# Performance work log

Measured on AMD Instinct MI355X. Metric: run time of the kernel, lower is better.

## Reference

```python
import jax, jax.numpy as jnp
import numpy as np
import math

B, T, C = 4, 2048, 1024
N_HEADS = 16
D_HEAD = C // N_HEADS


def _rope_tables(d_head, max_seq_len):
    half = d_head // 2
    theta = 1.0 / (10000.0 ** (jnp.arange(half, dtype=jnp.float32) / half))
    pos = jnp.arange(max_seq_len, dtype=jnp.float32)
    freqs = jnp.outer(pos, theta)  # [S, half]
    cos = jnp.concatenate([jnp.cos(freqs), jnp.cos(freqs)], axis=-1)  # [S, d_head]
    sin = jnp.concatenate([jnp.sin(freqs), jnp.sin(freqs)], axis=-1)
    return cos, sin


def _rotate_half(x):
    d = x.shape[-1] // 2
    return jnp.concatenate([-x[..., d:], x[..., :d]], axis=-1)


def _apply_rope(x, cos, sin):
    # x: [B, H, T, d_head]; cos/sin: [T, d_head] broadcast over B,H
    return x * cos[None, None] + _rotate_half(x) * sin[None, None]


def setup_inputs() -> dict:
    key = jax.random.key(0)
    k1, k2, k3 = jax.random.split(key, 3)
    x = jax.random.normal(k1, (B, T, C), dtype=jnp.float32)
    W_qkv = jax.random.normal(k2, (C, 3 * C), dtype=jnp.float32) * (1.0 / math.sqrt(C))
    W_proj = jax.random.normal(k3, (C, C), dtype=jnp.float32) * (1.0 / math.sqrt(C))
    return {"x": x, "W_qkv": W_qkv, "W_proj": W_proj}


def reference(x, W_qkv, W_proj):
    b, t, c = x.shape
    qkv = x @ W_qkv  # [B, T, 3C]
    q, k, v = jnp.split(qkv, 3, axis=-1)

    def reshape(z):
        return z.reshape(b, t, N_HEADS, D_HEAD).transpose(0, 2, 1, 3)  # [B,H,T,dh]

    q, k, v = reshape(q), reshape(k), reshape(v)

    cos, sin = _rope_tables(D_HEAD, t)
    q = _apply_rope(q, cos, sin)
    k = _apply_rope(k, cos, sin)

    scale = 1.0 / math.sqrt(D_HEAD)
    att = jnp.einsum('bhqd,bhkd->bhqk', q, k) * scale  # [B,H,T,T]
    causal = jnp.tril(jnp.ones((t, t), dtype=bool))
    att = jnp.where(causal[None, None], att, -jnp.inf)
    att = jax.nn.softmax(att, axis=-1)
    out = jnp.einsum('bhqk,bhkd->bhqd', att, v)  # [B,H,T,dh]
    out = out.transpose(0, 2, 1, 3).reshape(b, t, c)
    return out @ W_proj
```

## Files before the change

### kernel.cpp

```cpp
#include <hip/hip_runtime.h>
#include <stdint.h>

#define Bz 4
#define Tz 2048
#define Cz 1024
#define NHz 16
#define DHz 64
#define Mz (Bz*Tz)

typedef unsigned short u16;
typedef __attribute__((ext_vector_type(8))) short short8;
typedef __attribute__((ext_vector_type(8))) unsigned short ushort8v;
typedef __attribute__((ext_vector_type(4))) unsigned short u16x4;
typedef __attribute__((ext_vector_type(4))) float f32x4;
typedef __attribute__((ext_vector_type(2))) unsigned int uint2v;

__device__ __forceinline__ float bf2f(u16 u){
  union { unsigned int i; float f; } v; v.i = ((unsigned int)u) << 16; return v.f;
}
__device__ __forceinline__ u16 f2bf(float f){
  union { float f; unsigned int i; } v; v.f = f;
  unsigned int r = v.i + 0x7FFFu + ((v.i >> 16) & 1u);
  return (u16)(r >> 16);
}

__global__ void k_prep(const float* __restrict__ x,     u16* __restrict__ xb,
                       const float* __restrict__ Wqkv,  u16* __restrict__ wqt,
                       const float* __restrict__ Wproj, u16* __restrict__ wpt,
                       float* __restrict__ cosT, float* __restrict__ sinT){
  __shared__ float tile[32][33];
  const int blk = blockIdx.x;
  const int tid = threadIdx.x;
  if (blk < 8192){
    int i = blk*256 + tid;
    float4 v = ((const float4*)x)[i];
    u16x4 o;
    o[0] = f2bf(v.x); o[1] = f2bf(v.y); o[2] = f2bf(v.z); o[3] = f2bf(v.w);
    *(u16x4*)(xb + (size_t)i*4) = o;
  } else if (blk < 12288){
    const float* W; u16* Wt; int K, N, bx, by;
    if (blk < 11264){ int b2 = blk - 8192;  W = Wqkv;  Wt = wqt; K = 1024; N = 3072; bx = b2 % 96; by = b2 / 96; }
    else            { int b2 = blk - 11264; W = Wproj; Wt = wpt; K = 1024; N = 1024; bx = b2 % 32; by = b2 / 32; }
    const int n0 = bx*32, k0 = by*32;
    const int tx = tid & 31, ty = tid >> 5;
    #pragma unroll
    for (int i = 0; i < 32; i += 8)
      tile[ty+i][tx] = W[(size_t)(k0+ty+i)*N + n0 + tx];
    __syncthreads();
    #pragma unroll
    for (int i = 0; i < 32; i += 8)
      Wt[(size_t)(n0+ty+i)*K + k0 + tx] = f2bf(tile[tx][ty+i]);
  } else {
    int idx = (blk - 12288)*256 + tid;
    int t = idx >> 5, i = idx & 31;
    float theta = exp2f(-(float)i * (13.287712379549449f / 32.0f));
    float ang = (float)t * theta;
    cosT[idx] = cosf(ang);
    sinT[idx] = sinf(ang);
  }
}

#define GLDS(src, dstE) __builtin_amdgcn_global_load_lds( \
    (const __attribute__((address_space(1))) unsigned int*)(src), \
    (__attribute__((address_space(3))) unsigned int*)((u16*)lds + (dstE)), 16, 0, 0)

template<int Nn, int Kk, bool ROPE>
__global__ __launch_bounds__(256, 4) void k_gemmdb(const u16* __restrict__ A, const u16* __restrict__ Bt,
                        void* __restrict__ Cout, u16* __restrict__ vTout,
                        const float* __restrict__ cosT, const float* __restrict__ sinT){
  __shared__ u16 lds[2][16384];
  constexpr int NT = Kk/64;
  const int bm = blockIdx.x, bn = blockIdx.y;
  const int tid = threadIdx.x, lane = tid & 63, w = tid >> 6;
  const int wm = (w >> 1)*64, wn = (w & 1)*64;
  const int g = lane >> 4, r = lane & 15;

  const int srow8 = lane >> 3;
  const int sslot = (lane & 7) ^ srow8;
  const u16* asrc = A  + (size_t)(bm*128 + w*32 + srow8)*Kk + sslot*8;
  const u16* bsrc = Bt + (size_t)(bn*128 + w*32 + srow8)*Kk + sslot*8;
  const int dA = w*2048 + lane*8;
  const int dB = 8192 + w*2048 + lane*8;

  int a_off[4][2], b_off[4][2];
  #pragma unroll
  for (int i = 0; i < 4; ++i)
    #pragma unroll
    for (int kc = 0; kc < 2; ++kc){
      int row = wm + i*16 + r;
      a_off[i][kc] = (row*128 + kc*64 + g*16) ^ ((r & 7) << 4);
      int rowb = wn + i*16 + r;
      b_off[i][kc] = 16384 + ((rowb*128 + kc*64 + g*16) ^ ((r & 7) << 4));
    }

  f32x4 acc[4][4] = {};

#define STG(t, bi) do{ \
    const size_t ko_ = (size_t)(t)*64; \
    const int be_ = (bi)*16384; \
    GLDS(asrc + ko_,                 be_ + dA);        \
    GLDS(asrc + ko_ +  8*(size_t)Kk, be_ + dA + 512);  \
    GLDS(asrc + ko_ + 16*(size_t)Kk, be_ + dA + 1024); \
    GLDS(asrc + ko_ + 24*(size_t)Kk, be_ + dA + 1536); \
    GLDS(bsrc + ko_,                 be_ + dB);        \
    GLDS(bsrc + ko_ +  8*(size_t)Kk, be_ + dB + 512);  \
    GLDS(bsrc + ko_ + 16*(size_t)Kk, be_ + dB + 1024); \
    GLDS(bsrc + ko_ + 24*(size_t)Kk, be_ + dB + 1536); \
  }while(0)

  STG(0, 0);
  asm volatile("s_waitcnt vmcnt(0)" ::: "memory");
  __builtin_amdgcn_s_barrier();

  int buf = 0;
  #pragma unroll 1
  for (int t = 0; t < NT; ++t){
    if (t + 1 < NT) STG(t+1, buf^1);
    const char* Lb = (const char*)lds + buf*32768;
    short8 af[4][2], bf[4][2];
    #pragma unroll
    for (int i = 0; i < 4; ++i)
      #pragma unroll
      for (int kc = 0; kc < 2; ++kc){
        af[i][kc] = *(const short8*)(Lb + a_off[i][kc]);
        bf[i][kc] = *(const short8*)(Lb + b_off[i][kc]);
      }
    __builtin_amdgcn_s_setprio(1);
    #pragma unroll
    for (int i = 0; i < 4; ++i)
      #pragma unroll
      for (int j = 0; j < 4; ++j){
        acc[i][j] = __builtin_amdgcn_mfma_f32_16x16x32_bf16(af[i][0], bf[j][0], acc[i][j], 0,0,0);
        acc[i][j] = __builtin_amdgcn_mfma_f32_16x16x32_bf16(af[i][1], bf[j][1], acc[i][j], 0,0,0);
      }
    __builtin_amdgcn_s_setprio(0);
    if (t + 1 < NT){
      asm volatile("s_waitcnt vmcnt(0)" ::: "memory");
      __builtin_amdgcn_s_barrier();
      buf ^= 1;
    }
  }
#undef STG

  const int nbase = bn*128 + wn;
  if (ROPE && nbase >= 2048){
    const int b = bm >> 4;
    const int h = (nbase >> 6) & 15;
    #pragma unroll
    for (int ri = 0; ri < 4; ++ri){
      const int m0 = bm*128 + wm + ri*16 + 4*g;
      const int t0 = m0 & (Tz-1);
      #pragma unroll
      for (int cj = 0; cj < 4; ++cj){
        const int d = cj*16 + r;
        u16x4 o;
        #pragma unroll
        for (int jj = 0; jj < 4; ++jj) o[jj] = f2bf(acc[ri][cj][jj]);
        *(u16x4*)(vTout + ((size_t)((b*16 + h)*64 + d))*2048 + t0) = o;
      }
    }
  } else if (ROPE){
    const float qs = (nbase < 1024) ? 0.18033688011112042f : 1.0f;
    #pragma unroll
    for (int ri = 0; ri < 4; ++ri)
      #pragma unroll
      for (int jj = 0; jj < 4; ++jj){
        const int m = bm*128 + wm + ri*16 + 4*g + jj;
        const int t = m & (Tz-1);
        #pragma unroll
        for (int cj = 0; cj < 2; ++cj){
          const int ch = cj*16 + r;
          float cv = cosT[t*32 + ch];
          float sv = sinT[t*32 + ch];
          float lo = acc[ri][cj][jj], hi = acc[ri][cj+2][jj];
          ((u16*)Cout)[(size_t)m*Nn + nbase + ch]      = f2bf((lo*cv - hi*sv)*qs);
          ((u16*)Cout)[(size_t)m*Nn + nbase + ch + 32] = f2bf((hi*cv + lo*sv)*qs);
        }
      }
  } else {
    #pragma unroll
    for (int ri = 0; ri < 4; ++ri)
      #pragma unroll
      for (int cj = 0; cj < 4; ++cj)
        #pragma unroll
        for (int jj = 0; jj < 4; ++jj){
          const size_t m = bm*128 + wm + ri*16 + 4*g + jj;
          const size_t n = (size_t)nbase + cj*16 + r;
          ((float*)Cout)[m*Nn + n] = acc[ri][cj][jj];
        }
  }
}

__global__ __launch_bounds__(512) void k_attn2(const u16* __restrict__ qkv,
                                               const u16* __restrict__ vT,
                                               u16* __restrict__ att){
  __shared__ u16 K_lds[2*4096];
  __shared__ u16 V_lds[2*4096];
  __shared__ u16 P_lds[8*16*72];

  const int bh = blockIdx.x;
  const int b = bh >> 4, h = bh & 15;
  const int qt = 15 - blockIdx.y;
  const int tid = threadIdx.x;
  const int w = tid >> 6;
  const int lane = tid & 63;
  const int g = lane >> 4;
  const int ql = lane & 15;
  u16* Pw = P_lds + w*16*72;

  const int srow  = lane >> 3;
  const int sslot = (lane & 7) ^ srow;
  const u16* ksrc = qkv + ((size_t)(b*Tz + 8*w + srow))*3072 + 1024 + h*64 + sslot*8;
  const u16* vsrc = vT  + ((size_t)bh*64 + 8*w + srow)*2048 + sslot*8;
  u16* kdst = K_lds + w*512 + lane*8;
  u16* vdst = V_lds + w*512 + lane*8;

  short8 ones;
  #pragma unroll
  for (int i = 0; i < 8; ++i) ones[i] = (short)0x3F80;

  int fofs[4][2];
  #pragma unroll
  for (int t = 0; t < 4; ++t){
    int row = 16*t + ql;
    fofs[t][0] = (row*128 + 16*g)      ^ ((row & 7) << 4);
    fofs[t][1] = (row*128 + 64 + 16*g) ^ ((row & 7) << 4);
  }

  const int qr0w = qt*128 + w*16;
  const int nt = 2*qt + 2;

  const u16* qsrc = qkv + (size_t)(b*Tz + qr0w + ql)*3072 + h*64;
  short8 qf0 = *(const short8*)(qsrc + g*8);
  short8 qf1 = *(const short8*)(qsrc + 32 + g*8);

  f32x4 acc[4] = {{0,0,0,0},{0,0,0,0},{0,0,0,0},{0,0,0,0}};
  f32x4 accl = {0,0,0,0};

  __builtin_amdgcn_global_load_lds(
    (const __attribute__((address_space(1))) unsigned int*)(ksrc),
    (__attribute__((address_space(3))) unsigned int*)(kdst), 16, 0, 0);
  __builtin_amdgcn_global_load_lds(
    (const __attribute__((address_space(1))) unsigned int*)(vsrc),
    (__attribute__((address_space(3))) unsigned int*)(vdst), 16, 0, 0);
  __syncthreads();

  #pragma unroll 2
  for (int kt = 0; kt < nt; ++kt){
    const int buf = kt & 1;
    if (kt + 1 < nt){
      __builtin_amdgcn_global_load_lds(
        (const __attribute__((address_space(1))) unsigned int*)(ksrc + (size_t)(kt+1)*64*3072),
        (__attribute__((address_space(3))) unsigned int*)(kdst + (buf^1)*4096), 16, 0, 0);
      __builtin_amdgcn_global_load_lds(
        (const __attribute__((address_space(1))) unsigned int*)(vsrc + (kt+1)*64),
        (__attribute__((address_space(3))) unsigned int*)(vdst + (buf^1)*4096), 16, 0, 0);
    }
    const char* Kb = (const char*)(K_lds + buf*4096);
    const char* Vb = (const char*)(V_lds + buf*4096);
    const int kv0 = kt*64;

    f32x4 st[4];
    __builtin_amdgcn_s_setprio(1);
    #pragma unroll
    for (int t = 0; t < 4; ++t){
      short8 kf0 = *(const short8*)(Kb + fofs[t][0]);
      short8 kf1 = *(const short8*)(Kb + fofs[t][1]);
      f32x4 z = {0,0,0,0};
      z = __builtin_amdgcn_mfma_f32_16x16x32_bf16(kf0, qf0, z, 0, 0, 0);
      z = __builtin_amdgcn_mfma_f32_16x16x32_bf16(kf1, qf1, z, 0, 0, 0);
      st[t] = z;
    }
    __builtin_amdgcn_s_setprio(0);

    if (kv0 + 63 > qr0w){
      const int qg = qr0w + ql;
      #pragma unroll
      for (int t = 0; t < 4; ++t)
        #pragma unroll
        for (int j = 0; j < 4; ++j)
          if (kv0 + 16*t + 4*g + j > qg) st[t][j] = -1e30f;
    }

    #pragma unroll
    for (int t = 0; t < 4; ++t){
      float p0, p1, p2, p3;
      asm("v_exp_f32 %0, %1" : "=v"(p0) : "v"(st[t][0]));
      asm("v_exp_f32 %0, %1" : "=v"(p1) : "v"(st[t][1]));
      asm("v_exp_f32 %0, %1" : "=v"(p2) : "v"(st[t][2]));
      asm("v_exp_f32 %0, %1" : "=v"(p3) : "v"(st[t][3]));
      unsigned int lov, hiv;
      asm("v_cvt_pk_bf16_f32 %0, %1, %2" : "=v"(lov) : "v"(p0), "v"(p1));
      asm("v_cvt_pk_bf16_f32 %0, %1, %2" : "=v"(hiv) : "v"(p2), "v"(p3));
      uint2v pv; pv[0] = lov; pv[1] = hiv;
      *(uint2v*)((char*)Pw + ql*144 + (16*t + 4*g)*2) = pv;
    }

    short8 pf0 = *(const short8*)((char*)Pw + ql*144 + 16*g);
    short8 pf1 = *(const short8*)((char*)Pw + ql*144 + 64 + 16*g);
    __builtin_amdgcn_s_setprio(1);
    accl = __builtin_amdgcn_mfma_f32_16x16x32_bf16(pf0, ones, accl, 0, 0, 0);
    accl = __builtin_amdgcn_mfma_f32_16x16x32_bf16(pf1, ones, accl, 0, 0, 0);
    #pragma unroll
    for (int dt = 0; dt < 4; ++dt){
      short8 vf0 = *(const short8*)(Vb + fofs[dt][0]);
      short8 vf1 = *(const short8*)(Vb + fofs[dt][1]);
      acc[dt] = __builtin_amdgcn_mfma_f32_16x16x32_bf16(pf0, vf0, acc[dt], 0, 0, 0);
      acc[dt] = __builtin_amdgcn_mfma_f32_16x16x32_bf16(pf1, vf1, acc[dt], 0, 0, 0);
    }
    __builtin_amdgcn_s_setprio(0);
    __syncthreads();
  }

  float lj[4];
  #pragma unroll
  for (int j = 0; j < 4; ++j) lj[j] = 1.0f / accl[j];
  #pragma unroll
  for (int dt = 0; dt < 4; ++dt)
    #pragma unroll
    for (int j = 0; j < 4; ++j)
      att[(size_t)(b*Tz + qr0w + 4*g + j)*Cz + h*64 + dt*16 + ql] = f2bf(acc[dt][j]*lj[j]);
}


extern "C" void kernel_launch(void* const* d_in, const int* in_sizes, int n_in,
                              void* d_out, int out_size, void* d_ws, size_t ws_size,
                              hipStream_t stream){
  const float* x     = (const float*)d_in[0];
  const float* Wqkv  = (const float*)d_in[1];
  const float* Wproj = (const float*)d_in[2];
  float* out = (float*)d_out;
  char* ws = (char*)d_ws;

  u16*  xb   = (u16*)(ws);
  u16*  wqt  = (u16*)(ws + 16777216);
  u16*  wpt  = (u16*)(ws + 23068672);
  u16*  qkv  = (u16*)(ws + 25165824);
  u16*  vTr  = (u16*)(ws + 75497472);
  float* cosT = (float*)(ws + 92274688);
  float* sinT = (float*)(ws + 92536832);

  k_prep<<<12544, 256, 0, stream>>>(x, xb, Wqkv, wqt, Wproj, wpt, cosT, sinT);

  k_gemmdb<3072, 1024, true><<<dim3(Mz/128, 3072/128), 256, 0, stream>>>(
      xb, wqt, qkv, vTr, cosT, sinT);
  k_attn2<<<dim3(Bz*NHz, 16), 512, 0, stream>>>(qkv, vTr, xb);
  k_gemmdb<1024, 1024, false><<<dim3(Mz/128, 1024/128), 256, 0, stream>>>(
      xb, wpt, out, nullptr, nullptr, nullptr);
}
```

Before: 147.8 us.

## Software-pipeline attention loop by deferring PV MFMA to next iteration

Restructures the flash-attention K/V loop so the P·V and row-sum MFMAs for tile kt-1 run at the start of iteration kt, before the barrier. The K/V prefetch for the next tile is issued after that barrier, so the global-to-LDS copy has a full iteration of work (the next PV plus QK) to hide behind. An epilogue after the loop handles the last tile, and the loop unroll drops from 2 to 1. The cost is extra live registers for the carried P fragments and a slightly more complex buffer-reuse schedule.

```diff
diff --git a/kernel.cpp b/kernel.cpp
--- a/kernel.cpp
+++ b/kernel.cpp
@@ -236,30 +236,44 @@
 
   f32x4 acc[4] = {{0,0,0,0},{0,0,0,0},{0,0,0,0},{0,0,0,0}};
   f32x4 accl = {0,0,0,0};
-
-  __builtin_amdgcn_global_load_lds(
-    (const __attribute__((address_space(1))) unsigned int*)(ksrc),
-    (__attribute__((address_space(3))) unsigned int*)(kdst), 16, 0, 0);
-  __builtin_amdgcn_global_load_lds(
-    (const __attribute__((address_space(1))) unsigned int*)(vsrc),
-    (__attribute__((address_space(3))) unsigned int*)(vdst), 16, 0, 0);
-  __syncthreads();
-
-  #pragma unroll 2
+  short8 pf0, pf1;
+
+#define STG_KV(kt_, bi_) do{ \
+    __builtin_amdgcn_global_load_lds( \
+      (const __attribute__((address_space(1))) unsigned int*)(ksrc + (size_t)(kt_)*64*3072), \
+      (__attribute__((address_space(3))) unsigned int*)(kdst + (bi_)*4096), 16, 0, 0); \
+    __builtin_amdgcn_global_load_lds( \
+      (const __attribute__((address_space(1))) unsigned int*)(vsrc + (kt_)*64), \
+      (__attribute__((address_space(3))) unsigned int*)(vdst + (bi_)*4096), 16, 0, 0); \
+  }while(0)
+
+  STG_KV(0, 0);
+
+  #pragma unroll 1
   for (int kt = 0; kt < nt; ++kt){
-    const int buf = kt & 1;
-    if (kt + 1 < nt){
-      __builtin_amdgcn_global_load_lds(
-        (const __attribute__((address_space(1))) unsigned int*)(ksrc + (size_t)(kt+1)*64*3072),
-        (__attribute__((address_space(3))) unsigned int*)(kdst + (buf^1)*4096), 16, 0, 0);
-      __builtin_amdgcn_global_load_lds(
-        (const __attribute__((address_space(1))) unsigned int*)(vsrc + (kt+1)*64),
-        (__attribute__((address_space(3))) unsigned int*)(vdst + (buf^1)*4096), 16, 0, 0);
-    }
-    const char* Kb = (const char*)(K_lds + buf*4096);
-    const char* Vb = (const char*)(V_lds + buf*4096);
+    const int cur = kt & 1;
+
+    if (kt > 0){
+      const char* Vb = (const char*)(V_lds + (cur^1)*4096);
+      __builtin_amdgcn_s_setprio(1);
+      accl = __builtin_amdgcn_mfma_f32_16x16x32_bf16(pf0, ones, accl, 0, 0, 0);
+      accl = __builtin_amdgcn_mfma_f32_16x16x32_bf16(pf1, ones, accl, 0, 0, 0);
+      #pragma unroll
+      for (int dt = 0; dt < 4; ++dt){
+        short8 vf0 = *(const short8*)(Vb + fofs[dt][0]);
+        short8 vf1 = *(const short8*)(Vb + fofs[dt][1]);
+        acc[dt] = __builtin_amdgcn_mfma_f32_16x16x32_bf16(pf0, vf0, acc[dt], 0, 0, 0);
+        acc[dt] = __builtin_amdgcn_mfma_f32_16x16x32_bf16(pf1, vf1, acc[dt], 0, 0, 0);
+      }
+      __builtin_amdgcn_s_setprio(0);
+    }
+
+    __syncthreads();
+
+    if (kt + 1 < nt) STG_KV(kt+1, cur^1);
+
+    const char* Kb = (const char*)(K_lds + cur*4096);
     const int kv0 = kt*64;
-
     f32x4 st[4];
     __builtin_amdgcn_s_setprio(1);
     #pragma unroll
@@ -295,9 +309,12 @@
       uint2v pv; pv[0] = lov; pv[1] = hiv;
       *(uint2v*)((char*)Pw + ql*144 + (16*t + 4*g)*2) = pv;
     }
-
-    short8 pf0 = *(const short8*)((char*)Pw + ql*144 + 16*g);
-    short8 pf1 = *(const short8*)((char*)Pw + ql*144 + 64 + 16*g);
+    pf0 = *(const short8*)((char*)Pw + ql*144 + 16*g);
+    pf1 = *(const short8*)((char*)Pw + ql*144 + 64 + 16*g);
+  }
+
+  {
+    const char* Vb = (const char*)(V_lds + ((nt-1) & 1)*4096);
     __builtin_amdgcn_s_setprio(1);
     accl = __builtin_amdgcn_mfma_f32_16x16x32_bf16(pf0, ones, accl, 0, 0, 0);
     accl = __builtin_amdgcn_mfma_f32_16x16x32_bf16(pf1, ones, accl, 0, 0, 0);
@@ -309,8 +326,8 @@
       acc[dt] = __builtin_amdgcn_mfma_f32_16x16x32_bf16(pf1, vf1, acc[dt], 0, 0, 0);
     }
     __builtin_amdgcn_s_setprio(0);
-    __syncthreads();
-  }
+  }
+#undef STG_KV
 
   float lj[4];
   #pragma unroll
```

New measurement: 148.3 us. About the same (+0.4%).
